# Kernel optimization log

Hardware: AMD Instinct MI355X
Metric: run time of the kernel (lower is better)

The kernel has to match this reference:

```python
import jax, jax.numpy as jnp
import numpy as np

S, B, H = 2048, 32, 1024

def setup_inputs() -> dict:
    key = jax.random.key(0)
    k1, k2, k3 = jax.random.split(key, 3)
    hidden = jax.random.normal(k1, (1, B, H), dtype=jnp.float32)
    encoder_outputs = jax.random.normal(k2, (S, B, H), dtype=jnp.float32)
    W = jax.random.normal(k3, (H, H), dtype=jnp.float32) * (1.0 / np.sqrt(H))
    b = jnp.zeros((H,), dtype=jnp.float32)
    return {"hidden": hidden, "encoder_outputs": encoder_outputs, "W": W, "b": b}

def reference(hidden, encoder_outputs, W, b):
    # method == 'general': energy[b,i] = hidden[0,b] . (W @ enc[i,b] + bias)
    # proj: [S, B, H] = enc @ W^T + b  (nn.Linear convention: y = x W^T + b)
    proj = jnp.einsum('sbh,kh->sbk', encoder_outputs, W) + b
    # scores: [B, S]
    scores = jnp.einsum('bh,sbh->bs', hidden[0], proj)
    attn = jax.nn.softmax(scores, axis=1)
    return attn[:, None, :]  # [B, 1, S]
```

## Files before the change

### kernel.cpp

```cpp
#include <hip/hip_runtime.h>
#include <math.h>

#define H 1024
#define S 2048
#define B 32

typedef float floatx4 __attribute__((ext_vector_type(4)));

template <bool NT>
__device__ __forceinline__ float4 ld4(const float4* p) {
    if constexpr (NT) {
        floatx4 t = __builtin_nontemporal_load(reinterpret_cast<const floatx4*>(p));
        float4 r; r.x = t.x; r.y = t.y; r.z = t.z; r.w = t.w;
        return r;
    } else {
        return *p;
    }
}

__global__ void __launch_bounds__(512)
proj_hidden_kernel(const float* __restrict__ hidden,
                   const float* __restrict__ W,
                   float* __restrict__ v) {
    __shared__ float hs[2][H];
    __shared__ float part[32][2][64];
    const int hc = blockIdx.x & 15;
    const int bg = blockIdx.x >> 4;
    const int hq = threadIdx.x & 15;
    const int kg = threadIdx.x >> 4;

    for (int i = threadIdx.x; i < 2 * H; i += 512)
        hs[i >> 10][i & 1023] = hidden[(bg * 2 + (i >> 10)) * H + (i & 1023)];
    __syncthreads();

    const int h = hc * 64 + hq * 4;
    float4 a0 = {0.f, 0.f, 0.f, 0.f};
    float4 a1 = {0.f, 0.f, 0.f, 0.f};
#pragma unroll 4
    for (int kk = 0; kk < 32; ++kk) {
        const int k = kg + 32 * kk;
        const float h0 = hs[0][k];
        const float h1 = hs[1][k];
        const float4 w = *reinterpret_cast<const float4*>(W + (size_t)k * H + h);
        a0.x = fmaf(h0, w.x, a0.x); a0.y = fmaf(h0, w.y, a0.y);
        a0.z = fmaf(h0, w.z, a0.z); a0.w = fmaf(h0, w.w, a0.w);
        a1.x = fmaf(h1, w.x, a1.x); a1.y = fmaf(h1, w.y, a1.y);
        a1.z = fmaf(h1, w.z, a1.z); a1.w = fmaf(h1, w.w, a1.w);
    }
    *reinterpret_cast<float4*>(&part[kg][0][hq * 4]) = a0;
    *reinterpret_cast<float4*>(&part[kg][1][hq * 4]) = a1;
    __syncthreads();

    if (threadIdx.x < 128) {
        const int bb = threadIdx.x >> 6;
        const int c  = threadIdx.x & 63;
        float sum = 0.f;
#pragma unroll 8
        for (int g = 0; g < 32; ++g) sum += part[g][bb][c];
        v[(bg * 2 + bb) * H + hc * 64 + c] = sum;
    }
}

template <bool NT>
__device__ __forceinline__ void accum_rows(const float4* e0, const float4* e1,
                                           const float4* e2, const float4* e3,
                                           const float4* vb, int k,
                                           float& a0, float& a1,
                                           float& a2, float& a3) {
#pragma unroll 4
    for (int j = 0; j < 16; ++j) {
        const int f = k + 16 * j;
        const float4 w  = vb[f];
        const float4 x0 = ld4<NT>(e0 + f);
        const float4 x1 = ld4<NT>(e1 + f);
        const float4 x2 = ld4<NT>(e2 + f);
        const float4 x3 = ld4<NT>(e3 + f);
        a0 = fmaf(x0.x, w.x, fmaf(x0.y, w.y, fmaf(x0.z, w.z, fmaf(x0.w, w.w, a0))));
        a1 = fmaf(x1.x, w.x, fmaf(x1.y, w.y, fmaf(x1.z, w.z, fmaf(x1.w, w.w, a1))));
        a2 = fmaf(x2.x, w.x, fmaf(x2.y, w.y, fmaf(x2.z, w.z, fmaf(x2.w, w.w, a2))));
        a3 = fmaf(x3.x, w.x, fmaf(x3.y, w.y, fmaf(x3.z, w.z, fmaf(x3.w, w.w, a3))));
    }
}

__global__ void __launch_bounds__(512)
scores_kernel(const float* __restrict__ enc,
              const float* __restrict__ v,
              float* __restrict__ scores) {
    const int s0 = blockIdx.x * 4;
    const int b  = threadIdx.x >> 4;
    const int k  = threadIdx.x & 15;

    const float4* e0 = reinterpret_cast<const float4*>(enc + ((size_t)(s0 + 0) * B + b) * H);
    const float4* e1 = reinterpret_cast<const float4*>(enc + ((size_t)(s0 + 1) * B + b) * H);
    const float4* e2 = reinterpret_cast<const float4*>(enc + ((size_t)(s0 + 2) * B + b) * H);
    const float4* e3 = reinterpret_cast<const float4*>(enc + ((size_t)(s0 + 3) * B + b) * H);
    const float4* vb = reinterpret_cast<const float4*>(v + (size_t)b * H);

    float a0 = 0.f, a1 = 0.f, a2 = 0.f, a3 = 0.f;
    if (b < 28) {
        accum_rows<false>(e0, e1, e2, e3, vb, k, a0, a1, a2, a3);
    } else {
        accum_rows<true>(e0, e1, e2, e3, vb, k, a0, a1, a2, a3);
    }
#pragma unroll
    for (int off = 8; off > 0; off >>= 1) {
        a0 += __shfl_down(a0, off, 16);
        a1 += __shfl_down(a1, off, 16);
        a2 += __shfl_down(a2, off, 16);
        a3 += __shfl_down(a3, off, 16);
    }
    if (k == 0) {
        float4 r = {a0, a1, a2, a3};
        *reinterpret_cast<float4*>(scores + (size_t)b * S + s0) = r;
    }
}

__global__ void __launch_bounds__(256)
softmax_kernel(const float* __restrict__ scores,
               float* __restrict__ out) {
    const int b    = blockIdx.x;
    const int tid  = threadIdx.x;
    const int wave = tid >> 6;
    const int lane = tid & 63;

    __shared__ float wmax[4];
    __shared__ float wsum[4];

    float x[8];
    float m = -INFINITY;
#pragma unroll
    for (int i = 0; i < 8; ++i) {
        x[i] = scores[(size_t)b * S + tid + i * 256];
        m = fmaxf(m, x[i]);
    }
#pragma unroll
    for (int off = 32; off > 0; off >>= 1)
        m = fmaxf(m, __shfl_down(m, off, 64));
    if (lane == 0) wmax[wave] = m;
    __syncthreads();
    m = fmaxf(fmaxf(wmax[0], wmax[1]), fmaxf(wmax[2], wmax[3]));

    float sum = 0.f;
#pragma unroll
    for (int i = 0; i < 8; ++i) {
        x[i] = __expf(x[i] - m);
        sum += x[i];
    }
#pragma unroll
    for (int off = 32; off > 0; off >>= 1)
        sum += __shfl_down(sum, off, 64);
    if (lane == 0) wsum[wave] = sum;
    __syncthreads();
    sum = (wsum[0] + wsum[1]) + (wsum[2] + wsum[3]);

    const float inv = 1.0f / sum;
#pragma unroll
    for (int i = 0; i < 8; ++i) {
        out[(size_t)b * S + tid + i * 256] = x[i] * inv;
    }
}

extern "C" void kernel_launch(void* const* d_in, const int* in_sizes, int n_in,
                              void* d_out, int out_size, void* d_ws, size_t ws_size,
                              hipStream_t stream) {
    const float* hidden = (const float*)d_in[0];
    const float* enc    = (const float*)d_in[1];
    const float* W      = (const float*)d_in[2];

    float* v      = (float*)d_ws;
    float* scores = v + (size_t)B * H;
    float* out    = (float*)d_out;

    proj_hidden_kernel<<<256, 512, 0, stream>>>(hidden, W, v);
    scores_kernel<<<S / 4, 512, 0, stream>>>(enc, v, scores);
    softmax_kernel<<<B, 256, 0, stream>>>(scores, out);
}
```

Measured before the change: 54.39 us.

## Cache v slice in registers and process eight sequence rows per block

The scores kernel now loads each thread's 16 float4 values of the projected hidden vector into registers once, then loops over eight sequence positions in pairs instead of four positions at once. The grid shrinks to S/8 blocks. This is meant to remove repeated loads of v from cache for every row group and to amortise per-block setup. In exchange it uses more registers, keeps only two rows of loads in flight per iteration, and writes scores with scalar stores instead of float4.

Result: slower. 56.00 us (+3.0%).

```diff
diff --git a/kernel.cpp b/kernel.cpp
--- a/kernel.cpp
+++ b/kernel.cpp
@@ -62,23 +62,18 @@
 }
 
 template <bool NT>
-__device__ __forceinline__ void accum_rows(const float4* e0, const float4* e1,
-                                           const float4* e2, const float4* e3,
-                                           const float4* vb, int k,
-                                           float& a0, float& a1,
-                                           float& a2, float& a3) {
-#pragma unroll 4
+__device__ __forceinline__ void accum_pair(const float4* __restrict__ e0,
+                                           const float4* __restrict__ e1,
+                                           const float4 vr[16], int k,
+                                           float& a0, float& a1) {
+#pragma unroll
     for (int j = 0; j < 16; ++j) {
         const int f = k + 16 * j;
-        const float4 w  = vb[f];
         const float4 x0 = ld4<NT>(e0 + f);
         const float4 x1 = ld4<NT>(e1 + f);
-        const float4 x2 = ld4<NT>(e2 + f);
-        const float4 x3 = ld4<NT>(e3 + f);
+        const float4 w = vr[j];
         a0 = fmaf(x0.x, w.x, fmaf(x0.y, w.y, fmaf(x0.z, w.z, fmaf(x0.w, w.w, a0))));
         a1 = fmaf(x1.x, w.x, fmaf(x1.y, w.y, fmaf(x1.z, w.z, fmaf(x1.w, w.w, a1))));
-        a2 = fmaf(x2.x, w.x, fmaf(x2.y, w.y, fmaf(x2.z, w.z, fmaf(x2.w, w.w, a2))));
-        a3 = fmaf(x3.x, w.x, fmaf(x3.y, w.y, fmaf(x3.z, w.z, fmaf(x3.w, w.w, a3))));
     }
 }
 
@@ -86,32 +81,32 @@
 scores_kernel(const float* __restrict__ enc,
               const float* __restrict__ v,
               float* __restrict__ scores) {
-    const int s0 = blockIdx.x * 4;
+    const int s0 = blockIdx.x * 8;
     const int b  = threadIdx.x >> 4;
     const int k  = threadIdx.x & 15;
 
-    const float4* e0 = reinterpret_cast<const float4*>(enc + ((size_t)(s0 + 0) * B + b) * H);
-    const float4* e1 = reinterpret_cast<const float4*>(enc + ((size_t)(s0 + 1) * B + b) * H);
-    const float4* e2 = reinterpret_cast<const float4*>(enc + ((size_t)(s0 + 2) * B + b) * H);
-    const float4* e3 = reinterpret_cast<const float4*>(enc + ((size_t)(s0 + 3) * B + b) * H);
     const float4* vb = reinterpret_cast<const float4*>(v + (size_t)b * H);
+    float4 vr[16];
+#pragma unroll
+    for (int j = 0; j < 16; ++j) vr[j] = vb[k + 16 * j];
 
-    float a0 = 0.f, a1 = 0.f, a2 = 0.f, a3 = 0.f;
-    if (b < 28) {
-        accum_rows<false>(e0, e1, e2, e3, vb, k, a0, a1, a2, a3);
-    } else {
-        accum_rows<true>(e0, e1, e2, e3, vb, k, a0, a1, a2, a3);
-    }
+    for (int i = 0; i < 8; i += 2) {
+        const float4* e0 = reinterpret_cast<const float4*>(enc + ((size_t)(s0 + i + 0) * B + b) * H);
+        const float4* e1 = reinterpret_cast<const float4*>(enc + ((size_t)(s0 + i + 1) * B + b) * H);
+
+        float a0 = 0.f, a1 = 0.f;
+        if (b < 28) accum_pair<false>(e0, e1, vr, k, a0, a1);
+        else        accum_pair<true >(e0, e1, vr, k, a0, a1);
+
 #pragma unroll
-    for (int off = 8; off > 0; off >>= 1) {
-        a0 += __shfl_down(a0, off, 16);
-        a1 += __shfl_down(a1, off, 16);
-        a2 += __shfl_down(a2, off, 16);
-        a3 += __shfl_down(a3, off, 16);
-    }
-    if (k == 0) {
-        float4 r = {a0, a1, a2, a3};
-        *reinterpret_cast<float4*>(scores + (size_t)b * S + s0) = r;
+        for (int off = 8; off > 0; off >>= 1) {
+            a0 += __shfl_down(a0, off, 16);
+            a1 += __shfl_down(a1, off, 16);
+        }
+        if (k == 0) {
+            float* sp = scores + (size_t)b * S + s0 + i;
+            sp[0] = a0; sp[1] = a1;
+        }
     }
 }
 
@@ -172,6 +167,6 @@
     float* out    = (float*)d_out;
 
     proj_hidden_kernel<<<256, 512, 0, stream>>>(hidden, W, v);
-    scores_kernel<<<S / 4, 512, 0, stream>>>(enc, v, scores);
+    scores_kernel<<<S / 8, 512, 0, stream>>>(enc, v, scores);
     softmax_kernel<<<B, 256, 0, stream>>>(scores, out);
 }
```
